# Optimization experiments

Hardware: AMD Instinct MI355X
Metric: run time of the kernel (lower is better)

Reference implementation:

```python
import jax, jax.numpy as jnp
import numpy as np

DEPTH = 128
NEG_MAX = -jnp.finfo(jnp.float32).max


def setup_inputs() -> dict:
    key = jax.random.key(0)
    ks = jax.random.split(key, 10)
    B, S, F, C = 16, 2048, 512, 1000
    x = jax.random.normal(ks[0], (B, S, F), dtype=jnp.float32)
    attention_mask = jax.random.randint(ks[1], (B, S, S), 0, 2) == 1
    s = 1.0 / np.sqrt(F)
    Wq = jax.random.uniform(ks[2], (F, DEPTH), jnp.float32, -s, s)
    bq = jax.random.uniform(ks[3], (DEPTH,), jnp.float32, -s, s)
    Wk = jax.random.uniform(ks[4], (F, DEPTH), jnp.float32, -s, s)
    bk = jax.random.uniform(ks[5], (DEPTH,), jnp.float32, -s, s)
    Wv = jax.random.uniform(ks[6], (F, DEPTH), jnp.float32, -s, s)
    bv = jax.random.uniform(ks[7], (DEPTH,), jnp.float32, -s, s)
    sl = 1.0 / np.sqrt(DEPTH)
    Wl = jax.random.uniform(ks[8], (DEPTH, C), jnp.float32, -sl, sl)
    bl = jax.random.uniform(ks[9], (C,), jnp.float32, -sl, sl)
    return {"x": x, "attention_mask": attention_mask,
            "Wq": Wq, "bq": bq, "Wk": Wk, "bk": bk,
            "Wv": Wv, "bv": bv, "Wl": Wl, "bl": bl}


def reference(x, attention_mask, Wq, bq, Wk, bk, Wv, bv, Wl, bl):
    # x: [B, S, F]; single-head attention with depth=128
    q = (x @ Wq + bq) * (DEPTH ** -0.5)          # [B, S, D] (is_scaled_dot_product)
    k = x @ Wk + bk                               # [B, S, D]
    v = x @ Wv + bv                               # [B, S, D]
    logit = jnp.einsum('bsd,btd->bst', q, k)      # [B, S, S]
    # masked_fill_(mask, -float_max) then added to logits
    logit = logit + jnp.where(attention_mask, NEG_MAX, 0.0)
    attn = jax.nn.softmax(logit, axis=2)
    out = jnp.einsum('bst,btd->bsd', attn, v)     # [B, S, D]
    out = out @ Wl + bl                           # [B, S, C]
    return out.mean(axis=1)                       # [B, C]
```

## Files before the change

kernel.cpp:

```cpp
#include <hip/hip_runtime.h>
#include <stdint.h>

#define BB 16
#define SS 2048
#define FF 512
#define DD 128
#define CC 1000

typedef __attribute__((ext_vector_type(8))) short bf16x8;
typedef __attribute__((ext_vector_type(4))) float f32x4;

__device__ __forceinline__ unsigned short f2bf(float f) {
  unsigned x;
  __builtin_memcpy(&x, &f, 4);
  x = x + 0x7FFFu + ((x >> 16) & 1u);
  return (unsigned short)(x >> 16);
}
__device__ __forceinline__ float bf2f(unsigned short u) {
  unsigned x = ((unsigned)u) << 16;
  float f;
  __builtin_memcpy(&f, &x, 4);
  return f;
}
__device__ __forceinline__ unsigned pk2(float a, float b) {
  return (unsigned)f2bf(a) | ((unsigned)f2bf(b) << 16);
}

#define WS_PK   0
#define WS_Q    8388608
#define WS_K    16777216
#define WS_V    25165824
#define WS_WT   33554432
#define WS_WGP  33947648
#define WS_END  42336256

__global__ __launch_bounds__(256) void k_prep(const void* __restrict__ mask,
                                              const float* __restrict__ Wq,
                                              const float* __restrict__ Wk,
                                              const float* __restrict__ Wv,
                                              unsigned short* __restrict__ wt,
                                              unsigned* __restrict__ pk) {
  __shared__ unsigned red;
  const int tid = threadIdx.x;
  if (tid == 0) red = 0;
  __syncthreads();
  {
    unsigned a = 0;
    const unsigned* m32 = (const unsigned*)mask;
#pragma unroll
    for (int j = 0; j < 4; ++j) a |= m32[tid * 4 + j] & 0xFFFFFF00u;
    if (a) atomicOr(&red, 1u);
  }
  __syncthreads();
  const bool isInt = (red == 0);

  const long long base = (long long)blockIdx.x * 32768;
  for (int it = 0; it < 128; ++it) {
    long long e = base + it * 256 + tid;
    int val;
    if (isInt) val = ((const int*)mask)[e];
    else       val = ((const unsigned char*)mask)[e];
    unsigned long long bal = __ballot(val != 0);
    if ((tid & 31) == 0)
      pk[e >> 5] = (unsigned)((tid & 63) ? (bal >> 32) : bal);
  }

  if (blockIdx.x < 768) {
    int idx = blockIdx.x * 256 + tid;
    int ty = idx >> 16;
    int o = idx & 65535;
    int d = o >> 9, f = o & 511;
    const float* W = ty == 0 ? Wq : (ty == 1 ? Wk : Wv);
    wt[idx] = f2bf(W[f * DD + d]);
  }
}

__global__ __launch_bounds__(256) void k_proj(const float* __restrict__ xg,
                                              const unsigned short* __restrict__ wtg,
                                              const float* __restrict__ bq,
                                              const float* __restrict__ bk,
                                              const float* __restrict__ bv,
                                              unsigned short* __restrict__ qo,
                                              unsigned short* __restrict__ ko,
                                              unsigned short* __restrict__ vo) {
  __shared__ __align__(16) char lA[8192];
  __shared__ __align__(16) char lB[8192];
  const int tid = threadIdx.x;
  const int lane = tid & 63;
  const int wv = tid >> 6;
  const int colL = lane & 15, quad = lane >> 4;
  const int blk = blockIdx.x, ty = blockIdx.y;
  const float* bias = ty == 0 ? bq : (ty == 1 ? bk : bv);
  unsigned short* outp = ty == 0 ? qo : (ty == 1 ? ko : vo);
  const float scale = ty == 0 ? 0.08838834764831845f : 1.0f;
  const unsigned short* wbase = wtg + (size_t)ty * 65536;
  const int m0 = (wv & 1) * 64, n0 = (wv >> 1) * 64;

  f32x4 acc[4][4];
  const f32x4 z4 = {0.f, 0.f, 0.f, 0.f};
#pragma unroll
  for (int mi = 0; mi < 4; ++mi)
#pragma unroll
    for (int ni = 0; ni < 4; ++ni) acc[mi][ni] = z4;

  for (int ic = 0; ic < 16; ++ic) {
    const int k0 = ic * 32;
    uint4 va[2], vb[2];
#pragma unroll
    for (int rr = 0; rr < 2; ++rr) {
      int p = rr * 256 + tid;
      int row = p >> 2, c = p & 3;
      const float* xp = xg + (size_t)(blk * 128 + row) * FF + k0 + c * 8;
      float4 x0 = *(const float4*)xp;
      float4 x1 = *(const float4*)(xp + 4);
      va[rr].x = pk2(x0.x, x0.y); va[rr].y = pk2(x0.z, x0.w);
      va[rr].z = pk2(x1.x, x1.y); va[rr].w = pk2(x1.z, x1.w);
      vb[rr] = *(const uint4*)(wbase + (size_t)row * FF + k0 + c * 8);
    }
    __syncthreads();
#pragma unroll
    for (int rr = 0; rr < 2; ++rr) {
      int p = rr * 256 + tid;
      int row = p >> 2, c = p & 3;
      int phys = c ^ ((row >> 1) & 3);
      *(uint4*)(lA + row * 64 + phys * 16) = va[rr];
      *(uint4*)(lB + row * 64 + phys * 16) = vb[rr];
    }
    __syncthreads();
    bf16x8 af[4], bfr[4];
#pragma unroll
    for (int mi = 0; mi < 4; ++mi) {
      int ar = m0 + mi * 16 + colL;
      int phys = quad ^ ((ar >> 1) & 3);
      af[mi] = *(const bf16x8*)(lA + ar * 64 + phys * 16);
    }
#pragma unroll
    for (int ni = 0; ni < 4; ++ni) {
      int br = n0 + ni * 16 + colL;
      int phys = quad ^ ((br >> 1) & 3);
      bfr[ni] = *(const bf16x8*)(lB + br * 64 + phys * 16);
    }
#pragma unroll
    for (int mi = 0; mi < 4; ++mi)
#pragma unroll
      for (int ni = 0; ni < 4; ++ni)
        acc[mi][ni] = __builtin_amdgcn_mfma_f32_16x16x32_bf16(af[mi], bfr[ni], acc[mi][ni], 0, 0, 0);
  }
#pragma unroll
  for (int ni = 0; ni < 4; ++ni) {
    int col = n0 + ni * 16 + colL;
    float bval = bias[col];
#pragma unroll
    for (int mi = 0; mi < 4; ++mi) {
#pragma unroll
      for (int r = 0; r < 4; ++r) {
        int row = blk * 128 + m0 + mi * 16 + quad * 4 + r;
        float val = (acc[mi][ni][r] + bval) * scale;
        outp[(size_t)row * DD + col] = f2bf(val);
      }
    }
  }
}

__global__ __launch_bounds__(512, 2) void k_fatt(const unsigned short* __restrict__ qg,
                                                 const unsigned short* __restrict__ kg,
                                                 const unsigned* __restrict__ pk,
                                                 float* __restrict__ wgp) {
  extern __shared__ __align__(16) char smem[];
  unsigned short* pt = (unsigned short*)smem;
  char* kt = smem + 131072;
  unsigned* mk = (unsigned*)(smem + 147456);
  float* zfin = (float*)(smem + 155776);
  float* zinvl = (float*)(smem + 155904);

  const int tid = threadIdx.x;
  const int lane = tid & 63, wv = tid >> 6;
  const int colL = lane & 15, quad = lane >> 4;
  const int wr = wv & 1, wq = wv >> 1;
  const int r0 = blockIdx.x * 32;
  const int b = blockIdx.y;

  for (int i = tid; i < 2048; i += 512) {
    int row = i >> 6, w = i & 63;
    mk[row * 65 + w] = pk[((size_t)b * SS + r0 + row) * 64 + w];
  }
  if (tid < 32) zfin[tid] = 0.f;

  bf16x8 qf[4];
  {
    int qrow = r0 + wr * 16 + colL;
    const unsigned short* qp = qg + ((size_t)b * SS + qrow) * DD + quad * 8;
#pragma unroll
    for (int kk = 0; kk < 4; ++kk) qf[kk] = *(const bf16x8*)(qp + kk * 32);
  }

  const int krow = tid >> 3, kc8 = tid & 7;
  const unsigned short* kbase = kg + ((size_t)b * SS + krow) * DD;
  const int kswz0 = (kc8 ^ (krow & 7)) * 16;
  const int kswz1 = ((kc8 + 8) ^ (krow & 7)) * 16;

  uint4 kreg0 = *(const uint4*)(kbase + kc8 * 8);
  uint4 kreg1 = *(const uint4*)(kbase + kc8 * 8 + 64);
  *(uint4*)(kt + krow * 256 + kswz0) = kreg0;
  *(uint4*)(kt + krow * 256 + kswz1) = kreg1;
  __syncthreads();

  float z[4] = {0.f, 0.f, 0.f, 0.f};
  const int tb = wq * 16 + colL;

  for (int c = 0; c < 32; ++c) {
    if (c < 31) {
      const unsigned short* kb2 = kbase + (size_t)(c + 1) * 64 * DD;
      kreg0 = *(const uint4*)(kb2 + kc8 * 8);
      kreg1 = *(const uint4*)(kb2 + kc8 * 8 + 64);
    }
    bf16x8 bb[4];
#pragma unroll
    for (int kk = 0; kk < 4; ++kk) {
      int phys = (kk * 4 + quad) ^ (tb & 7);
      bb[kk] = *(const bf16x8*)(kt + tb * 256 + phys * 16);
    }
    f32x4 acc = {0.f, 0.f, 0.f, 0.f};
    acc = __builtin_amdgcn_mfma_f32_16x16x32_bf16(qf[0], bb[0], acc, 0, 0, 0);
    acc = __builtin_amdgcn_mfma_f32_16x16x32_bf16(qf[1], bb[1], acc, 0, 0, 0);
    acc = __builtin_amdgcn_mfma_f32_16x16x32_bf16(qf[2], bb[2], acc, 0, 0, 0);
    acc = __builtin_amdgcn_mfma_f32_16x16x32_bf16(qf[3], bb[3], acc, 0, 0, 0);
    int tl = c * 64 + tb;
    int widx = tl >> 5, wb = tl & 31;
#pragma unroll
    for (int r = 0; r < 4; ++r) {
      int row_l = wr * 16 + quad * 4 + r;
      unsigned mw = mk[row_l * 65 + widx];
      float e = ((mw >> wb) & 1u) ? 0.f : __expf(fminf(acc[r], 80.f));
      z[r] += e;
      pt[row_l * 2048 + (tl ^ ((row_l & 7) << 3))] = f2bf(e);
    }
    if (c < 31) {
      __syncthreads();
      *(uint4*)(kt + krow * 256 + kswz0) = kreg0;
      *(uint4*)(kt + krow * 256 + kswz1) = kreg1;
      __syncthreads();
    }
  }

#pragma unroll
  for (int r = 0; r < 4; ++r) {
    float s = z[r];
    s += __shfl_xor(s, 1, 64);
    s += __shfl_xor(s, 2, 64);
    s += __shfl_xor(s, 4, 64);
    s += __shfl_xor(s, 8, 64);
    if (colL == 0) atomicAdd(&zfin[wr * 16 + quad * 4 + r], s);
  }
  __syncthreads();
  if (tid < 32) zinvl[tid] = 1.0f / fmaxf(zfin[tid], 1e-30f);
  __syncthreads();

  {
    const int t0 = tid * 4;
    float a0 = 0.f, a1 = 0.f, a2 = 0.f, a3 = 0.f;
#pragma unroll 8
    for (int r = 0; r < 32; ++r) {
      const unsigned short* pr = pt + r * 2048 + (t0 ^ ((r & 7) << 3));
      ushort4 pv = *(const ushort4*)pr;
      float zi = zinvl[r];
      a0 += bf2f(pv.x) * zi;
      a1 += bf2f(pv.y) * zi;
      a2 += bf2f(pv.z) * zi;
      a3 += bf2f(pv.w) * zi;
    }
    float4 o4;
    o4.x = a0; o4.y = a1; o4.z = a2; o4.w = a3;
    *(float4*)(wgp + ((size_t)b * 64 + blockIdx.x) * SS + t0) = o4;
  }
}

__global__ __launch_bounds__(1024) void k_tail(const float* __restrict__ wgp,
                                               const unsigned short* __restrict__ vg,
                                               const float* __restrict__ Wl,
                                               const float* __restrict__ bl,
                                               float* __restrict__ outp) {
  __shared__ float ws2[2048];
  __shared__ float yp[8][128];
  __shared__ float ys[128];
  const int tid = threadIdx.x;
  const int b = blockIdx.x;

  {
    float s0 = 0.f, s1 = 0.f;
    const float* wp = wgp + ((size_t)b * 64) * SS + tid * 2;
#pragma unroll 8
    for (int rg = 0; rg < 64; ++rg) {
      s0 += wp[rg * SS];
      s1 += wp[rg * SS + 1];
    }
    ws2[tid * 2] = s0;
    ws2[tid * 2 + 1] = s1;
  }
  __syncthreads();

  {
    const int d = tid & 127, tg = tid >> 7;
    const int t0 = tg * 256;
    float p = 0.f;
    const unsigned short* vr = vg + ((size_t)b * SS + t0) * DD + d;
#pragma unroll 8
    for (int t = 0; t < 256; ++t) p += ws2[t0 + t] * bf2f(vr[(size_t)t * DD]);
    yp[tg][d] = p;
  }
  __syncthreads();
  if (tid < 128) {
    float a = 0.f;
#pragma unroll
    for (int g = 0; g < 8; ++g) a += yp[g][tid];
    ys[tid] = a * (1.0f / 2048.0f);
  }
  __syncthreads();

  if (tid < CC) {
    float a = bl[tid];
#pragma unroll 16
    for (int dd = 0; dd < DD; ++dd) a += ys[dd] * Wl[dd * CC + tid];
    outp[b * CC + tid] = a;
  }
}

extern "C" void kernel_launch(void* const* d_in, const int* in_sizes, int n_in,
                              void* d_out, int out_size, void* d_ws, size_t ws_size,
                              hipStream_t stream) {
  const void* ptr[10];
  for (int i = 0; i < 10; ++i) ptr[i] = (i < n_in) ? d_in[i] : nullptr;
  if (n_in == 10) {
    const void *px = 0, *pm = 0, *pWl = 0, *pbl = 0;
    const void* pW[3] = {0, 0, 0};
    const void* pb[3] = {0, 0, 0};
    int nW = 0, nb = 0;
    for (int i = 0; i < 10; ++i) {
      int s = in_sizes[i];
      if (s == 16777216) px = d_in[i];
      else if (s == 67108864) pm = d_in[i];
      else if (s == 128000) pWl = d_in[i];
      else if (s == 1000) pbl = d_in[i];
      else if (s == 65536 && nW < 3) pW[nW++] = d_in[i];
      else if (s == 128 && nb < 3) pb[nb++] = d_in[i];
    }
    if (px && pm && pWl && pbl && nW == 3 && nb == 3) {
      ptr[0] = px; ptr[1] = pm;
      ptr[2] = pW[0]; ptr[3] = pb[0];
      ptr[4] = pW[1]; ptr[5] = pb[1];
      ptr[6] = pW[2]; ptr[7] = pb[2];
      ptr[8] = pWl; ptr[9] = pbl;
    }
  }
  char* ws = (char*)d_ws;
  if (ws_size < (size_t)WS_END) return;
  unsigned* pk = (unsigned*)(ws + WS_PK);
  unsigned short* q  = (unsigned short*)(ws + WS_Q);
  unsigned short* k  = (unsigned short*)(ws + WS_K);
  unsigned short* v  = (unsigned short*)(ws + WS_V);
  unsigned short* wt = (unsigned short*)(ws + WS_WT);
  float* wgp = (float*)(ws + WS_WGP);

  k_prep<<<2048, 256, 0, stream>>>(ptr[1], (const float*)ptr[2], (const float*)ptr[4],
                                   (const float*)ptr[6], wt, pk);
  k_proj<<<dim3(256, 3), 256, 0, stream>>>((const float*)ptr[0], wt,
                                           (const float*)ptr[3], (const float*)ptr[5],
                                           (const float*)ptr[7], q, k, v);
  k_fatt<<<dim3(64, 16), 512, 156032, stream>>>(q, k, pk, wgp);
  k_tail<<<16, 1024, 0, stream>>>(wgp, v, (const float*)ptr[8], (const float*)ptr[9],
                                  (float*)d_out);
}
```

Before: 577.3 us.

## Fuse QKV projections per block and keep softmax probabilities in registers

k_proj now converts each 128-row x tile to bf16 once into a 128KB LDS buffer and loops over the Q, K and V weights inside a single block. Before, three separate block groups each re-read and re-converted x. k_fatt stops staging the 32x2048 probability tile in LDS. It keeps packed bf16 exponentials in 64 registers per thread, reduces the column sums with shuffles and LDS atomics, and double-buffers the K tile so one barrier per chunk is dropped. The trade-offs are higher register pressure in k_fatt, a large LDS footprint that limits k_proj to one block per CU, and 256 k_proj blocks with less parallelism.

Measured after the change: 625.3 us. +8.3%, slower.

```diff
diff --git a/kernel.cpp b/kernel.cpp
--- a/kernel.cpp
+++ b/kernel.cpp
@@ -83,80 +83,92 @@
                                               unsigned short* __restrict__ qo,
                                               unsigned short* __restrict__ ko,
                                               unsigned short* __restrict__ vo) {
-  __shared__ __align__(16) char lA[8192];
-  __shared__ __align__(16) char lB[8192];
+  extern __shared__ __align__(16) char smem[];
+  char* xA = smem;
+  char* lB = smem + 131072;
   const int tid = threadIdx.x;
   const int lane = tid & 63;
   const int wv = tid >> 6;
   const int colL = lane & 15, quad = lane >> 4;
-  const int blk = blockIdx.x, ty = blockIdx.y;
-  const float* bias = ty == 0 ? bq : (ty == 1 ? bk : bv);
-  unsigned short* outp = ty == 0 ? qo : (ty == 1 ? ko : vo);
-  const float scale = ty == 0 ? 0.08838834764831845f : 1.0f;
-  const unsigned short* wbase = wtg + (size_t)ty * 65536;
+  const int blk = blockIdx.x;
   const int m0 = (wv & 1) * 64, n0 = (wv >> 1) * 64;
 
-  f32x4 acc[4][4];
-  const f32x4 z4 = {0.f, 0.f, 0.f, 0.f};
-#pragma unroll
-  for (int mi = 0; mi < 4; ++mi)
-#pragma unroll
-    for (int ni = 0; ni < 4; ++ni) acc[mi][ni] = z4;
-
-  for (int ic = 0; ic < 16; ++ic) {
-    const int k0 = ic * 32;
-    uint4 va[2], vb[2];
-#pragma unroll
-    for (int rr = 0; rr < 2; ++rr) {
-      int p = rr * 256 + tid;
-      int row = p >> 2, c = p & 3;
-      const float* xp = xg + (size_t)(blk * 128 + row) * FF + k0 + c * 8;
-      float4 x0 = *(const float4*)xp;
-      float4 x1 = *(const float4*)(xp + 4);
-      va[rr].x = pk2(x0.x, x0.y); va[rr].y = pk2(x0.z, x0.w);
-      va[rr].z = pk2(x1.x, x1.y); va[rr].w = pk2(x1.z, x1.w);
-      vb[rr] = *(const uint4*)(wbase + (size_t)row * FF + k0 + c * 8);
-    }
-    __syncthreads();
-#pragma unroll
-    for (int rr = 0; rr < 2; ++rr) {
-      int p = rr * 256 + tid;
-      int row = p >> 2, c = p & 3;
-      int phys = c ^ ((row >> 1) & 3);
-      *(uint4*)(lA + row * 64 + phys * 16) = va[rr];
-      *(uint4*)(lB + row * 64 + phys * 16) = vb[rr];
-    }
-    __syncthreads();
-    bf16x8 af[4], bfr[4];
-#pragma unroll
-    for (int mi = 0; mi < 4; ++mi) {
-      int ar = m0 + mi * 16 + colL;
-      int phys = quad ^ ((ar >> 1) & 3);
-      af[mi] = *(const bf16x8*)(lA + ar * 64 + phys * 16);
+#pragma unroll 4
+  for (int it = 0; it < 32; ++it) {
+    int id = it * 256 + tid;
+    int row = id >> 6, c = id & 63;
+    const float* xp = xg + (size_t)(blk * 128 + row) * FF + c * 8;
+    float4 x0 = *(const float4*)xp;
+    float4 x1 = *(const float4*)(xp + 4);
+    uint4 w;
+    w.x = pk2(x0.x, x0.y); w.y = pk2(x0.z, x0.w);
+    w.z = pk2(x1.x, x1.y); w.w = pk2(x1.z, x1.w);
+    *(uint4*)(xA + row * 1024 + (c ^ (row & 63)) * 16) = w;
+  }
+
+  for (int ty = 0; ty < 3; ++ty) {
+    const float* bias = ty == 0 ? bq : (ty == 1 ? bk : bv);
+    unsigned short* outp = ty == 0 ? qo : (ty == 1 ? ko : vo);
+    const float scale = ty == 0 ? 0.08838834764831845f : 1.0f;
+    const unsigned short* wbase = wtg + (size_t)ty * 65536;
+
+    f32x4 acc[4][4];
+    const f32x4 z4 = {0.f, 0.f, 0.f, 0.f};
+#pragma unroll
+    for (int mi = 0; mi < 4; ++mi)
+#pragma unroll
+      for (int ni = 0; ni < 4; ++ni) acc[mi][ni] = z4;
+
+    for (int ic = 0; ic < 16; ++ic) {
+      const int k0 = ic * 32;
+      uint4 vb[2];
+#pragma unroll
+      for (int rr = 0; rr < 2; ++rr) {
+        int p = rr * 256 + tid;
+        int row = p >> 2, c = p & 3;
+        vb[rr] = *(const uint4*)(wbase + (size_t)row * FF + k0 + c * 8);
+      }
+      __syncthreads();
+#pragma unroll
+      for (int rr = 0; rr < 2; ++rr) {
+        int p = rr * 256 + tid;
+        int row = p >> 2, c = p & 3;
+        int phys = c ^ ((row >> 1) & 3);
+        *(uint4*)(lB + row * 64 + phys * 16) = vb[rr];
+      }
+      __syncthreads();
+      bf16x8 af[4], bfr[4];
+#pragma unroll
+      for (int mi = 0; mi < 4; ++mi) {
+        int ar = m0 + mi * 16 + colL;
+        int cch = ic * 4 + quad;
+        int phys = cch ^ (ar & 63);
+        af[mi] = *(const bf16x8*)(xA + ar * 1024 + phys * 16);
+      }
+#pragma unroll
+      for (int ni = 0; ni < 4; ++ni) {
+        int br = n0 + ni * 16 + colL;
+        int phys = quad ^ ((br >> 1) & 3);
+        bfr[ni] = *(const bf16x8*)(lB + br * 64 + phys * 16);
+      }
+#pragma unroll
+      for (int mi = 0; mi < 4; ++mi)
+#pragma unroll
+        for (int ni = 0; ni < 4; ++ni)
+          acc[mi][ni] = __builtin_amdgcn_mfma_f32_16x16x32_bf16(af[mi], bfr[ni], acc[mi][ni], 0, 0, 0);
     }
 #pragma unroll
     for (int ni = 0; ni < 4; ++ni) {
-      int br = n0 + ni * 16 + colL;
-      int phys = quad ^ ((br >> 1) & 3);
-      bfr[ni] = *(const bf16x8*)(lB + br * 64 + phys * 16);
-    }
-#pragma unroll
-    for (int mi = 0; mi < 4; ++mi)
-#pragma unroll
-      for (int ni = 0; ni < 4; ++ni)
-        acc[mi][ni] = __builtin_amdgcn_mfma_f32_16x16x32_bf16(af[mi], bfr[ni], acc[mi][ni], 0, 0, 0);
-  }
-#pragma unroll
-  for (int ni = 0; ni < 4; ++ni) {
-    int col = n0 + ni * 16 + colL;
-    float bval = bias[col];
-#pragma unroll
-    for (int mi = 0; mi < 4; ++mi) {
-#pragma unroll
-      for (int r = 0; r < 4; ++r) {
-        int row = blk * 128 + m0 + mi * 16 + quad * 4 + r;
-        float val = (acc[mi][ni][r] + bval) * scale;
-        outp[(size_t)row * DD + col] = f2bf(val);
+      int col = n0 + ni * 16 + colL;
+      float bval = bias[col];
+#pragma unroll
+      for (int mi = 0; mi < 4; ++mi) {
+#pragma unroll
+        for (int r = 0; r < 4; ++r) {
+          int row = blk * 128 + m0 + mi * 16 + quad * 4 + r;
+          float val = (acc[mi][ni][r] + bval) * scale;
+          outp[(size_t)row * DD + col] = f2bf(val);
+        }
       }
     }
   }
@@ -166,12 +178,11 @@
                                                  const unsigned short* __restrict__ kg,
                                                  const unsigned* __restrict__ pk,
                                                  float* __restrict__ wgp) {
-  extern __shared__ __align__(16) char smem[];
-  unsigned short* pt = (unsigned short*)smem;
-  char* kt = smem + 131072;
-  unsigned* mk = (unsigned*)(smem + 147456);
-  float* zfin = (float*)(smem + 155776);
-  float* zinvl = (float*)(smem + 155904);
+  __shared__ __align__(16) char kt[32768];
+  __shared__ unsigned mk[32 * 65];
+  __shared__ float wacc[2048];
+  __shared__ float zfin[32];
+  __shared__ float zinvl[32];
 
   const int tid = threadIdx.x;
   const int lane = tid & 63, wv = tid >> 6;
@@ -183,6 +194,7 @@
   for (int i = tid; i < 2048; i += 512) {
     int row = i >> 6, w = i & 63;
     mk[row * 65 + w] = pk[((size_t)b * SS + r0 + row) * 64 + w];
+    wacc[i] = 0.f;
   }
   if (tid < 32) zfin[tid] = 0.f;
 
@@ -199,46 +211,59 @@
   const int kswz0 = (kc8 ^ (krow & 7)) * 16;
   const int kswz1 = ((kc8 + 8) ^ (krow & 7)) * 16;
 
-  uint4 kreg0 = *(const uint4*)(kbase + kc8 * 8);
-  uint4 kreg1 = *(const uint4*)(kbase + kc8 * 8 + 64);
-  *(uint4*)(kt + krow * 256 + kswz0) = kreg0;
-  *(uint4*)(kt + krow * 256 + kswz1) = kreg1;
+  {
+    uint4 k0r = *(const uint4*)(kbase + kc8 * 8);
+    uint4 k1r = *(const uint4*)(kbase + kc8 * 8 + 64);
+    *(uint4*)(kt + krow * 256 + kswz0) = k0r;
+    *(uint4*)(kt + krow * 256 + kswz1) = k1r;
+  }
   __syncthreads();
 
   float z[4] = {0.f, 0.f, 0.f, 0.f};
+  unsigned estore[64];
   const int tb = wq * 16 + colL;
 
+#pragma unroll
   for (int c = 0; c < 32; ++c) {
+    uint4 k0r, k1r;
     if (c < 31) {
       const unsigned short* kb2 = kbase + (size_t)(c + 1) * 64 * DD;
-      kreg0 = *(const uint4*)(kb2 + kc8 * 8);
-      kreg1 = *(const uint4*)(kb2 + kc8 * 8 + 64);
-    }
+      k0r = *(const uint4*)(kb2 + kc8 * 8);
+      k1r = *(const uint4*)(kb2 + kc8 * 8 + 64);
+    }
+    const char* ktb = kt + (c & 1) * 16384;
     bf16x8 bb[4];
 #pragma unroll
     for (int kk = 0; kk < 4; ++kk) {
       int phys = (kk * 4 + quad) ^ (tb & 7);
-      bb[kk] = *(const bf16x8*)(kt + tb * 256 + phys * 16);
+      bb[kk] = *(const bf16x8*)(ktb + tb * 256 + phys * 16);
     }
     f32x4 acc = {0.f, 0.f, 0.f, 0.f};
     acc = __builtin_amdgcn_mfma_f32_16x16x32_bf16(qf[0], bb[0], acc, 0, 0, 0);
     acc = __builtin_amdgcn_mfma_f32_16x16x32_bf16(qf[1], bb[1], acc, 0, 0, 0);
     acc = __builtin_amdgcn_mfma_f32_16x16x32_bf16(qf[2], bb[2], acc, 0, 0, 0);
     acc = __builtin_amdgcn_mfma_f32_16x16x32_bf16(qf[3], bb[3], acc, 0, 0, 0);
-    int tl = c * 64 + tb;
-    int widx = tl >> 5, wb = tl & 31;
-#pragma unroll
-    for (int r = 0; r < 4; ++r) {
-      int row_l = wr * 16 + quad * 4 + r;
-      unsigned mw = mk[row_l * 65 + widx];
-      float e = ((mw >> wb) & 1u) ? 0.f : __expf(fminf(acc[r], 80.f));
-      z[r] += e;
-      pt[row_l * 2048 + (tl ^ ((row_l & 7) << 3))] = f2bf(e);
-    }
+    const int tl = c * 64 + tb;
+    const int widx = tl >> 5, wb = tl & 31;
+    const int rbase = wr * 16 + quad * 4;
+    float e0, e1, e2, e3;
+    {
+      unsigned mw0 = mk[(rbase + 0) * 65 + widx];
+      unsigned mw1 = mk[(rbase + 1) * 65 + widx];
+      unsigned mw2 = mk[(rbase + 2) * 65 + widx];
+      unsigned mw3 = mk[(rbase + 3) * 65 + widx];
+      e0 = ((mw0 >> wb) & 1u) ? 0.f : __expf(fminf(acc[0], 80.f));
+      e1 = ((mw1 >> wb) & 1u) ? 0.f : __expf(fminf(acc[1], 80.f));
+      e2 = ((mw2 >> wb) & 1u) ? 0.f : __expf(fminf(acc[2], 80.f));
+      e3 = ((mw3 >> wb) & 1u) ? 0.f : __expf(fminf(acc[3], 80.f));
+    }
+    z[0] += e0; z[1] += e1; z[2] += e2; z[3] += e3;
+    estore[c * 2]     = pk2(e0, e1);
+    estore[c * 2 + 1] = pk2(e2, e3);
     if (c < 31) {
-      __syncthreads();
-      *(uint4*)(kt + krow * 256 + kswz0) = kreg0;
-      *(uint4*)(kt + krow * 256 + kswz1) = kreg1;
+      char* ktn = kt + ((c + 1) & 1) * 16384;
+      *(uint4*)(ktn + krow * 256 + kswz0) = k0r;
+      *(uint4*)(ktn + krow * 256 + kswz1) = k1r;
       __syncthreads();
     }
   }
@@ -257,20 +282,24 @@
   __syncthreads();
 
   {
+    f32x4 zi = *(const f32x4*)(zinvl + wr * 16 + quad * 4);
+#pragma unroll
+    for (int c = 0; c < 32; ++c) {
+      unsigned u0 = estore[c * 2], u1 = estore[c * 2 + 1];
+      float cs = bf2f((unsigned short)(u0 & 0xFFFFu)) * zi[0]
+               + bf2f((unsigned short)(u0 >> 16))     * zi[1]
+               + bf2f((unsigned short)(u1 & 0xFFFFu)) * zi[2]
+               + bf2f((unsigned short)(u1 >> 16))     * zi[3];
+      cs += __shfl_xor(cs, 16, 64);
+      cs += __shfl_xor(cs, 32, 64);
+      if (quad == 0) atomicAdd(&wacc[c * 64 + wq * 16 + colL], cs);
+    }
+  }
+  __syncthreads();
+  {
     const int t0 = tid * 4;
-    float a0 = 0.f, a1 = 0.f, a2 = 0.f, a3 = 0.f;
-#pragma unroll 8
-    for (int r = 0; r < 32; ++r) {
-      const unsigned short* pr = pt + r * 2048 + (t0 ^ ((r & 7) << 3));
-      ushort4 pv = *(const ushort4*)pr;
-      float zi = zinvl[r];
-      a0 += bf2f(pv.x) * zi;
-      a1 += bf2f(pv.y) * zi;
-      a2 += bf2f(pv.z) * zi;
-      a3 += bf2f(pv.w) * zi;
-    }
     float4 o4;
-    o4.x = a0; o4.y = a1; o4.z = a2; o4.w = a3;
+    o4.x = wacc[t0]; o4.y = wacc[t0 + 1]; o4.z = wacc[t0 + 2]; o4.w = wacc[t0 + 3];
     *(float4*)(wgp + ((size_t)b * 64 + blockIdx.x) * SS + t0) = o4;
   }
 }
@@ -363,10 +392,10 @@
 
   k_prep<<<2048, 256, 0, stream>>>(ptr[1], (const float*)ptr[2], (const float*)ptr[4],
                                    (const float*)ptr[6], wt, pk);
-  k_proj<<<dim3(256, 3), 256, 0, stream>>>((const float*)ptr[0], wt,
-                                           (const float*)ptr[3], (const float*)ptr[5],
-                                           (const float*)ptr[7], q, k, v);
-  k_fatt<<<dim3(64, 16), 512, 156032, stream>>>(q, k, pk, wgp);
+  k_proj<<<256, 256, 139264, stream>>>((const float*)ptr[0], wt,
+                                       (const float*)ptr[3], (const float*)ptr[5],
+                                       (const float*)ptr[7], q, k, v);
+  k_fatt<<<dim3(64, 16), 512, 0, stream>>>(q, k, pk, wgp);
   k_tail<<<16, 1024, 0, stream>>>(wgp, v, (const float*)ptr[8], (const float*)ptr[9],
                                   (float*)d_out);
 }
```

## Recompute attention scores in a second pass instead of storing the P tile in LDS

Applied to the files above, without the earlier changes.

The fused attention kernel no longer stores the 32x2048 bf16 probability tile in shared memory. After the first pass computes the row normalisers, it reloads K and recomputes QK^T and exp in a second pass. Each column's normalised weights are accumulated on the fly through wave shuffles into a small fp32 column-sum buffer. This cuts LDS per block from about 156KB to about 41KB, so more blocks can be resident per CU, and it removes the scattered bf16 stores and the final row-reduction loop. In exchange the matrix-multiply, exp and K-load work is doubled.

Result: no change. 585.3 us (+1.4%).

```diff
diff --git a/kernel.cpp b/kernel.cpp
--- a/kernel.cpp
+++ b/kernel.cpp
@@ -166,12 +166,11 @@
                                                  const unsigned short* __restrict__ kg,
                                                  const unsigned* __restrict__ pk,
                                                  float* __restrict__ wgp) {
-  extern __shared__ __align__(16) char smem[];
-  unsigned short* pt = (unsigned short*)smem;
-  char* kt = smem + 131072;
-  unsigned* mk = (unsigned*)(smem + 147456);
-  float* zfin = (float*)(smem + 155776);
-  float* zinvl = (float*)(smem + 155904);
+  __shared__ __align__(16) char kt[16384];
+  __shared__ unsigned mk[32 * 65];
+  __shared__ float wacc2[2][2048];
+  __shared__ float zfin[32];
+  __shared__ float zinvl[32];
 
   const int tid = threadIdx.x;
   const int lane = tid & 63, wv = tid >> 6;
@@ -183,6 +182,8 @@
   for (int i = tid; i < 2048; i += 512) {
     int row = i >> 6, w = i & 63;
     mk[row * 65 + w] = pk[((size_t)b * SS + r0 + row) * 64 + w];
+    wacc2[0][i] = 0.f;
+    wacc2[1][i] = 0.f;
   }
   if (tid < 32) zfin[tid] = 0.f;
 
@@ -198,6 +199,8 @@
   const unsigned short* kbase = kg + ((size_t)b * SS + krow) * DD;
   const int kswz0 = (kc8 ^ (krow & 7)) * 16;
   const int kswz1 = ((kc8 + 8) ^ (krow & 7)) * 16;
+  const int tb = wq * 16 + colL;
+  const int rbase = wr * 16 + quad * 4;
 
   uint4 kreg0 = *(const uint4*)(kbase + kc8 * 8);
   uint4 kreg1 = *(const uint4*)(kbase + kc8 * 8 + 64);
@@ -206,8 +209,6 @@
   __syncthreads();
 
   float z[4] = {0.f, 0.f, 0.f, 0.f};
-  const int tb = wq * 16 + colL;
-
   for (int c = 0; c < 32; ++c) {
     if (c < 31) {
       const unsigned short* kb2 = kbase + (size_t)(c + 1) * 64 * DD;
@@ -225,15 +226,13 @@
     acc = __builtin_amdgcn_mfma_f32_16x16x32_bf16(qf[1], bb[1], acc, 0, 0, 0);
     acc = __builtin_amdgcn_mfma_f32_16x16x32_bf16(qf[2], bb[2], acc, 0, 0, 0);
     acc = __builtin_amdgcn_mfma_f32_16x16x32_bf16(qf[3], bb[3], acc, 0, 0, 0);
-    int tl = c * 64 + tb;
-    int widx = tl >> 5, wb = tl & 31;
+    const int tl = c * 64 + tb;
+    const int widx = tl >> 5, wb = tl & 31;
 #pragma unroll
     for (int r = 0; r < 4; ++r) {
-      int row_l = wr * 16 + quad * 4 + r;
-      unsigned mw = mk[row_l * 65 + widx];
+      unsigned mw = mk[(rbase + r) * 65 + widx];
       float e = ((mw >> wb) & 1u) ? 0.f : __expf(fminf(acc[r], 80.f));
       z[r] += e;
-      pt[row_l * 2048 + (tl ^ ((row_l & 7) << 3))] = f2bf(e);
     }
     if (c < 31) {
       __syncthreads();
@@ -256,21 +255,58 @@
   if (tid < 32) zinvl[tid] = 1.0f / fmaxf(zfin[tid], 1e-30f);
   __syncthreads();
 
+  const f32x4 zi = *(const f32x4*)(&zinvl[rbase]);
+
+  kreg0 = *(const uint4*)(kbase + kc8 * 8);
+  kreg1 = *(const uint4*)(kbase + kc8 * 8 + 64);
+  *(uint4*)(kt + krow * 256 + kswz0) = kreg0;
+  *(uint4*)(kt + krow * 256 + kswz1) = kreg1;
+  __syncthreads();
+
+  for (int c = 0; c < 32; ++c) {
+    if (c < 31) {
+      const unsigned short* kb2 = kbase + (size_t)(c + 1) * 64 * DD;
+      kreg0 = *(const uint4*)(kb2 + kc8 * 8);
+      kreg1 = *(const uint4*)(kb2 + kc8 * 8 + 64);
+    }
+    bf16x8 bb[4];
+#pragma unroll
+    for (int kk = 0; kk < 4; ++kk) {
+      int phys = (kk * 4 + quad) ^ (tb & 7);
+      bb[kk] = *(const bf16x8*)(kt + tb * 256 + phys * 16);
+    }
+    f32x4 acc = {0.f, 0.f, 0.f, 0.f};
+    acc = __builtin_amdgcn_mfma_f32_16x16x32_bf16(qf[0], bb[0], acc, 0, 0, 0);
+    acc = __builtin_amdgcn_mfma_f32_16x16x32_bf16(qf[1], bb[1], acc, 0, 0, 0);
+    acc = __builtin_amdgcn_mfma_f32_16x16x32_bf16(qf[2], bb[2], acc, 0, 0, 0);
+    acc = __builtin_amdgcn_mfma_f32_16x16x32_bf16(qf[3], bb[3], acc, 0, 0, 0);
+    const int tl = c * 64 + tb;
+    const int widx = tl >> 5, wb = tl & 31;
+    float cs = 0.f;
+#pragma unroll
+    for (int r = 0; r < 4; ++r) {
+      unsigned mw = mk[(rbase + r) * 65 + widx];
+      float e = ((mw >> wb) & 1u) ? 0.f : __expf(fminf(acc[r], 80.f));
+      cs += e * zi[r];
+    }
+    cs += __shfl_xor(cs, 16, 64);
+    cs += __shfl_xor(cs, 32, 64);
+    if (quad == 0) wacc2[wr][tl] += cs;
+    if (c < 31) {
+      __syncthreads();
+      *(uint4*)(kt + krow * 256 + kswz0) = kreg0;
+      *(uint4*)(kt + krow * 256 + kswz1) = kreg1;
+      __syncthreads();
+    }
+  }
+  __syncthreads();
   {
     const int t0 = tid * 4;
-    float a0 = 0.f, a1 = 0.f, a2 = 0.f, a3 = 0.f;
-#pragma unroll 8
-    for (int r = 0; r < 32; ++r) {
-      const unsigned short* pr = pt + r * 2048 + (t0 ^ ((r & 7) << 3));
-      ushort4 pv = *(const ushort4*)pr;
-      float zi = zinvl[r];
-      a0 += bf2f(pv.x) * zi;
-      a1 += bf2f(pv.y) * zi;
-      a2 += bf2f(pv.z) * zi;
-      a3 += bf2f(pv.w) * zi;
-    }
     float4 o4;
-    o4.x = a0; o4.y = a1; o4.z = a2; o4.w = a3;
+    o4.x = wacc2[0][t0]     + wacc2[1][t0];
+    o4.y = wacc2[0][t0 + 1] + wacc2[1][t0 + 1];
+    o4.z = wacc2[0][t0 + 2] + wacc2[1][t0 + 2];
+    o4.w = wacc2[0][t0 + 3] + wacc2[1][t0 + 3];
     *(float4*)(wgp + ((size_t)b * 64 + blockIdx.x) * SS + t0) = o4;
   }
 }
@@ -366,7 +402,7 @@
   k_proj<<<dim3(256, 3), 256, 0, stream>>>((const float*)ptr[0], wt,
                                            (const float*)ptr[3], (const float*)ptr[5],
                                            (const float*)ptr[7], q, k, v);
-  k_fatt<<<dim3(64, 16), 512, 156032, stream>>>(q, k, pk, wgp);
+  k_fatt<<<dim3(64, 16), 512, 0, stream>>>(q, k, pk, wgp);
   k_tail<<<16, 1024, 0, stream>>>(wgp, v, (const float*)ptr[8], (const float*)ptr[9],
                                   (float*)d_out);
 }
```

## Load K fragments directly from global into registers, drop LDS K staging

Applied to the files above, without the earlier changes.

Removes the shared-memory K tile and its two per-chunk barriers in the score loop. Each lane now reads its MFMA B fragments straight from global memory, with register double-buffering across chunks. Shared memory moves to static arrays, which shrinks the LDS footprint by the K tile. The risk is more global traffic, since each K row is now loaded redundantly by the two row-waves, and the loads are less coalesced.

Result: slower. 627.9 us (+8.8%).

```diff
diff --git a/kernel.cpp b/kernel.cpp
--- a/kernel.cpp
+++ b/kernel.cpp
@@ -166,12 +166,10 @@
                                                  const unsigned short* __restrict__ kg,
                                                  const unsigned* __restrict__ pk,
                                                  float* __restrict__ wgp) {
-  extern __shared__ __align__(16) char smem[];
-  unsigned short* pt = (unsigned short*)smem;
-  char* kt = smem + 131072;
-  unsigned* mk = (unsigned*)(smem + 147456);
-  float* zfin = (float*)(smem + 155776);
-  float* zinvl = (float*)(smem + 155904);
+  __shared__ __align__(16) unsigned short pt[32 * 2048];
+  __shared__ unsigned mk[32 * 65];
+  __shared__ float zfin[32];
+  __shared__ float zinvl[32];
 
   const int tid = threadIdx.x;
   const int lane = tid & 63, wv = tid >> 6;
@@ -193,55 +191,52 @@
 #pragma unroll
     for (int kk = 0; kk < 4; ++kk) qf[kk] = *(const bf16x8*)(qp + kk * 32);
   }
-
-  const int krow = tid >> 3, kc8 = tid & 7;
-  const unsigned short* kbase = kg + ((size_t)b * SS + krow) * DD;
-  const int kswz0 = (kc8 ^ (krow & 7)) * 16;
-  const int kswz1 = ((kc8 + 8) ^ (krow & 7)) * 16;
-
-  uint4 kreg0 = *(const uint4*)(kbase + kc8 * 8);
-  uint4 kreg1 = *(const uint4*)(kbase + kc8 * 8 + 64);
-  *(uint4*)(kt + krow * 256 + kswz0) = kreg0;
-  *(uint4*)(kt + krow * 256 + kswz1) = kreg1;
-  __syncthreads();
+  __syncthreads();
+
+  const int tb = wq * 16 + colL;
+  const int rbase = wr * 16 + quad * 4;
+  const unsigned short* kfb = kg + ((size_t)b * SS + tb) * DD + quad * 8;
 
   float z[4] = {0.f, 0.f, 0.f, 0.f};
-  const int tb = wq * 16 + colL;
-
-  for (int c = 0; c < 32; ++c) {
-    if (c < 31) {
-      const unsigned short* kb2 = kbase + (size_t)(c + 1) * 64 * DD;
-      kreg0 = *(const uint4*)(kb2 + kc8 * 8);
-      kreg1 = *(const uint4*)(kb2 + kc8 * 8 + 64);
-    }
-    bf16x8 bb[4];
-#pragma unroll
-    for (int kk = 0; kk < 4; ++kk) {
-      int phys = (kk * 4 + quad) ^ (tb & 7);
-      bb[kk] = *(const bf16x8*)(kt + tb * 256 + phys * 16);
-    }
-    f32x4 acc = {0.f, 0.f, 0.f, 0.f};
-    acc = __builtin_amdgcn_mfma_f32_16x16x32_bf16(qf[0], bb[0], acc, 0, 0, 0);
-    acc = __builtin_amdgcn_mfma_f32_16x16x32_bf16(qf[1], bb[1], acc, 0, 0, 0);
-    acc = __builtin_amdgcn_mfma_f32_16x16x32_bf16(qf[2], bb[2], acc, 0, 0, 0);
-    acc = __builtin_amdgcn_mfma_f32_16x16x32_bf16(qf[3], bb[3], acc, 0, 0, 0);
-    int tl = c * 64 + tb;
-    int widx = tl >> 5, wb = tl & 31;
-#pragma unroll
-    for (int r = 0; r < 4; ++r) {
-      int row_l = wr * 16 + quad * 4 + r;
-      unsigned mw = mk[row_l * 65 + widx];
-      float e = ((mw >> wb) & 1u) ? 0.f : __expf(fminf(acc[r], 80.f));
-      z[r] += e;
-      pt[row_l * 2048 + (tl ^ ((row_l & 7) << 3))] = f2bf(e);
-    }
-    if (c < 31) {
-      __syncthreads();
-      *(uint4*)(kt + krow * 256 + kswz0) = kreg0;
-      *(uint4*)(kt + krow * 256 + kswz1) = kreg1;
-      __syncthreads();
-    }
-  }
+
+#define LOADC(dst, c)                                            \
+  {                                                              \
+    const unsigned short* kp_ = kfb + (size_t)(c) * 64 * DD;     \
+    dst[0] = *(const bf16x8*)(kp_);                              \
+    dst[1] = *(const bf16x8*)(kp_ + 32);                         \
+    dst[2] = *(const bf16x8*)(kp_ + 64);                         \
+    dst[3] = *(const bf16x8*)(kp_ + 96);                         \
+  }
+
+#define COMPUTE(bbuf, c)                                                          \
+  {                                                                               \
+    f32x4 acc = {0.f, 0.f, 0.f, 0.f};                                             \
+    acc = __builtin_amdgcn_mfma_f32_16x16x32_bf16(qf[0], bbuf[0], acc, 0, 0, 0);  \
+    acc = __builtin_amdgcn_mfma_f32_16x16x32_bf16(qf[1], bbuf[1], acc, 0, 0, 0);  \
+    acc = __builtin_amdgcn_mfma_f32_16x16x32_bf16(qf[2], bbuf[2], acc, 0, 0, 0);  \
+    acc = __builtin_amdgcn_mfma_f32_16x16x32_bf16(qf[3], bbuf[3], acc, 0, 0, 0);  \
+    const int tl = (c) * 64 + tb;                                                 \
+    const int widx = tl >> 5, wb = tl & 31;                                       \
+    _Pragma("unroll")                                                             \
+    for (int r = 0; r < 4; ++r) {                                                 \
+      int row_l = rbase + r;                                                      \
+      unsigned mw = mk[row_l * 65 + widx];                                        \
+      float e = ((mw >> wb) & 1u) ? 0.f : __expf(fminf(acc[r], 80.f));            \
+      z[r] += e;                                                                  \
+      pt[row_l * 2048 + (tl ^ ((row_l & 7) << 3))] = f2bf(e);                     \
+    }                                                                             \
+  }
+
+  bf16x8 b0[4], b1[4];
+  LOADC(b0, 0);
+  for (int c = 0; c < 32; c += 2) {
+    LOADC(b1, c + 1);
+    COMPUTE(b0, c);
+    if (c + 2 < 32) LOADC(b0, c + 2);
+    COMPUTE(b1, c + 1);
+  }
+#undef LOADC
+#undef COMPUTE
 
 #pragma unroll
   for (int r = 0; r < 4; ++r) {
@@ -366,7 +361,7 @@
   k_proj<<<dim3(256, 3), 256, 0, stream>>>((const float*)ptr[0], wt,
                                            (const float*)ptr[3], (const float*)ptr[5],
                                            (const float*)ptr[7], q, k, v);
-  k_fatt<<<dim3(64, 16), 512, 156032, stream>>>(q, k, pk, wgp);
+  k_fatt<<<dim3(64, 16), 512, 0, stream>>>(q, k, pk, wgp);
   k_tail<<<16, 1024, 0, stream>>>(wgp, v, (const float*)ptr[8], (const float*)ptr[9],
                                   (float*)d_out);
 }
```
